# Performance work log

Hardware: AMD Instinct MI355X
Metric: run time of the kernel (lower is better)

Reference implementation:

```python
import jax, jax.numpy as jnp
import numpy as np

B, C, H, W = 4, 256, 128, 128


def setup_inputs() -> dict:
    key = jax.random.key(0)
    k1, k2, k3, k4 = jax.random.split(key, 4)
    x = jax.random.normal(k1, (B, C, H, W), dtype=jnp.float32)
    offset = jax.random.normal(k2, (B, 18, H, W), dtype=jnp.float32)
    # 1x1 conv weights, normal_init std=0.01, zero bias (mmcv normal_init default)
    w0 = jax.random.normal(k3, (C, C), dtype=jnp.float32) * 0.01
    b0 = jnp.zeros((C,), dtype=jnp.float32)
    w1 = jax.random.normal(k4, (C, C), dtype=jnp.float32) * 0.01
    b1 = jnp.zeros((C,), dtype=jnp.float32)
    return {"x": x, "offset": offset, "w0": w0, "b0": b0, "w1": w1, "b1": b1}


def _bilinear(x, py, px):
    # x: [B,C,H,W]; py,px: [B,H,W] fractional sample coords; zero outside bounds (DCN convention)
    Bb, Cc, Hh, Ww = x.shape
    y0 = jnp.floor(py)
    x0 = jnp.floor(px)
    wy = (py - y0)[:, None]  # [B,1,H,W]
    wx = (px - x0)[:, None]
    y0i = y0.astype(jnp.int32)
    x0i = x0.astype(jnp.int32)
    xf = x.reshape(Bb, Cc, Hh * Ww)

    def corner(yi, xi):
        valid = ((yi >= 0) & (yi < Hh) & (xi >= 0) & (xi < Ww)).astype(x.dtype)
        idx = (jnp.clip(yi, 0, Hh - 1) * Ww + jnp.clip(xi, 0, Ww - 1)).reshape(Bb, 1, Hh * Ww)
        v = jnp.take_along_axis(xf, idx, axis=2).reshape(Bb, Cc, Hh, Ww)
        return v * valid[:, None]

    v00 = corner(y0i, x0i)
    v01 = corner(y0i, x0i + 1)
    v10 = corner(y0i + 1, x0i)
    v11 = corner(y0i + 1, x0i + 1)
    return (v00 * (1 - wy) * (1 - wx) + v01 * (1 - wy) * wx
            + v10 * wy * (1 - wx) + v11 * wy * wx)


def _channel_norm(t):
    t = t - t.mean(axis=1, keepdims=True)
    return t / jnp.sqrt(jnp.sum(t * t, axis=1, keepdims=True) + 1e-5)


def reference(x, offset, w0, b0, w1, b1):
    Bb, Cc, Hh, Ww = x.shape
    ys = jnp.arange(Hh, dtype=x.dtype)[:, None]  # [H,1]
    xs = jnp.arange(Ww, dtype=x.dtype)[None, :]  # [1,W]
    # deformable 3x3 unfold fused with max over the 9 sample points
    q = None
    for k in range(9):
        kh, kw = k // 3 - 1, k % 3 - 1
        py = ys + kh + offset[:, 2 * k]      # [B,H,W]
        px = xs + kw + offset[:, 2 * k + 1]
        s = _bilinear(x, py, px)             # [B,C,H,W]
        q = s if q is None else jnp.maximum(q, s)
    query = jnp.einsum('oc,bchw->bohw', w0, q) + b0[None, :, None, None]
    key = jnp.einsum('oc,bchw->bohw', w1, x) + b1[None, :, None, None]
    out = jnp.sum(_channel_norm(query) * _channel_norm(key), axis=1, keepdims=True)
    return out  # [B,1,H,W]
```

## Files before the change

### kernel.cpp

```cpp
#include <hip/hip_runtime.h>
#include <math.h>
#include <float.h>

#define Bd 4
#define Cd 256
#define Hd 128
#define Wd 128
#define HW (Hd*Wd)

#define PX 128
#define KC 32
#define PXM 32
#define CSTR 264

typedef __attribute__((ext_vector_type(8))) short s16x8;
typedef __attribute__((ext_vector_type(4))) float f32x4;

__device__ __forceinline__ void bf16split(float v, ushort& h, ushort& lo_) {
  uint u = __builtin_bit_cast(uint, v);
  uint uh = u + 0x7FFFu + ((u >> 16) & 1u);
  ushort hh = (ushort)(uh >> 16);
  float hf = __builtin_bit_cast(float, (uint)hh << 16);
  float res = v - hf;
  uint r = __builtin_bit_cast(uint, res);
  uint rl = r + 0x7FFFu + ((r >> 16) & 1u);
  h = hh; lo_ = (ushort)(rl >> 16);
}

__global__ __launch_bounds__(256) void prep_w_k(
    const float* __restrict__ w0, const float* __restrict__ w1,
    ushort* __restrict__ wpk) {
  const int t    = blockIdx.x * 256 + threadIdx.x;
  const int lane = t & 63;
  const int tile = (t >> 6) & 15;
  const int kc   = (t >> 10) & 7;
  const int mat  = t >> 13;
  const float* wsrc = mat ? w1 : w0;
  const int o  = tile * 16 + (lane & 15);
  const int c0 = kc * 32 + (lane >> 4) * 8;
  ushort hi[8], lo[8];
#pragma unroll
  for (int j = 0; j < 8; ++j)
    bf16split(wsrc[o * Cd + c0 + j], hi[j], lo[j]);
  const size_t bh = ((((size_t)(mat * 2 + 0) * 8 + kc) * 16 + tile) * 64 + lane) * 8;
  const size_t bl = ((((size_t)(mat * 2 + 1) * 8 + kc) * 16 + tile) * 64 + lane) * 8;
#pragma unroll
  for (int j = 0; j < 8; ++j) { wpk[bh + j] = hi[j]; wpk[bl + j] = lo[j]; }
}

__global__ __launch_bounds__(256) void transpose_x_k(
    const float* __restrict__ x, float* __restrict__ xT) {
  __shared__ float t[32][33];
  const int b   = blockIdx.z;
  const int hw0 = blockIdx.x * 32;
  const int c0  = blockIdx.y * 32;
  const int tx = threadIdx.x & 31, ty = threadIdx.x >> 5;
  const float* xb  = x  + (size_t)b * Cd * HW;
  float*       xTb = xT + (size_t)b * HW * Cd;
#pragma unroll
  for (int i = 0; i < 32; i += 8)
    t[ty + i][tx] = xb[(size_t)(c0 + ty + i) * HW + hw0 + tx];
  __syncthreads();
#pragma unroll
  for (int i = 0; i < 32; i += 8)
    xTb[(size_t)(hw0 + ty + i) * Cd + c0 + tx] = t[tx][ty + i];
}

__device__ __forceinline__ void deform_job(
    int j, int pbase, const float* __restrict__ offb, uint* __restrict__ dstbase) {
  const int px = j / 9, k = j - px * 9;
  const int p = pbase + px;
  const int h = p >> 7, w = p & (Wd - 1);
  const float oy = offb[(2 * k) * HW + p];
  const float ox = offb[(2 * k + 1) * HW + p];
  const float py = (float)(h + k / 3 - 1) + oy;
  const float pxx = (float)(w + k % 3 - 1) + ox;
  const float y0f = floorf(py), x0f = floorf(pxx);
  const float wy = py - y0f, wx = pxx - x0f;
  const int y0 = (int)y0f, x0 = (int)x0f;
  const int y1 = y0 + 1,  x1 = x0 + 1;
  const float vy0 = (y0 >= 0 && y0 < Hd) ? 1.f : 0.f;
  const float vy1 = (y1 >= 0 && y1 < Hd) ? 1.f : 0.f;
  const float vx0 = (x0 >= 0 && x0 < Wd) ? 1.f : 0.f;
  const float vx1 = (x1 >= 0 && x1 < Wd) ? 1.f : 0.f;
  const int cy0 = min(max(y0, 0), Hd-1), cy1 = min(max(y1, 0), Hd-1);
  const int cx0 = min(max(x0, 0), Wd-1), cx1 = min(max(x1, 0), Wd-1);
  uint4 iv;
  iv.x = (uint)(cy0 * Wd + cx0) * Cd;
  iv.y = (uint)(cy0 * Wd + cx1) * Cd;
  iv.z = (uint)(cy1 * Wd + cx0) * Cd;
  iv.w = (uint)(cy1 * Wd + cx1) * Cd;
  float4 cv;
  cv.x = (1.f-wy)*(1.f-wx) * vy0*vx0;
  cv.y = (1.f-wy)*wx       * vy0*vx1;
  cv.z = wy*(1.f-wx)       * vy1*vx0;
  cv.w = wy*wx             * vy1*vx1;
  uint* d = dstbase + (size_t)(px * 9 + k) * 8;
  *(uint4*)d = iv;
  *(float4*)(d + 4) = cv;
}

__global__ __launch_bounds__(256) void merged_k(
    const float* __restrict__ xT, const float* __restrict__ off,
    const ushort* __restrict__ wpk,
    const float* __restrict__ b0, const float* __restrict__ b1,
    float* __restrict__ out) {
  __shared__ ushort act[4 * PXM * CSTR];
  __shared__ __align__(16) uint coef[4][8 * 9 * 8];

  const int bid = blockIdx.x;
  const int swz = (bid & 7) * 256 + (bid >> 3);
  const int b    = swz >> 9;
  const int tile = swz & 511;

  const int tid = threadIdx.x;
  const int l   = tid & 63, wv = tid >> 6;
  const int px0   = tile * PXM;
  const int pbase = px0 + wv * 8;

  const float* offb = off + (size_t)b * 18 * HW;

  deform_job(l, pbase, offb, &coef[wv][0]);
  if (l < 8) deform_job(64 + l, pbase, offb, &coef[wv][0]);
  __syncthreads();

  {
    const float* xTb = xT + (size_t)b * HW * Cd + l * 4;
    ushort* qh_base = act + 0 * PXM * CSTR;
    ushort* ql_base = act + 1 * PXM * CSTR;
#pragma unroll 2
    for (int pi = 0; pi < 8; ++pi) {
      float m0 = -FLT_MAX, m1 = -FLT_MAX, m2 = -FLT_MAX, m3 = -FLT_MAX;
#pragma unroll
      for (int k = 0; k < 9; ++k) {
        const uint* cp = &coef[wv][(pi * 9 + k) * 8];
        const uint4  iv = *(const uint4*)cp;
        const float4 cw = *(const float4*)(cp + 4);
        const float4 v00 = *(const float4*)(xTb + iv.x);
        const float4 v01 = *(const float4*)(xTb + iv.y);
        const float4 v10 = *(const float4*)(xTb + iv.z);
        const float4 v11 = *(const float4*)(xTb + iv.w);
        m0 = fmaxf(m0, fmaf(cw.x, v00.x, fmaf(cw.y, v01.x, fmaf(cw.z, v10.x, cw.w*v11.x))));
        m1 = fmaxf(m1, fmaf(cw.x, v00.y, fmaf(cw.y, v01.y, fmaf(cw.z, v10.y, cw.w*v11.y))));
        m2 = fmaxf(m2, fmaf(cw.x, v00.z, fmaf(cw.y, v01.z, fmaf(cw.z, v10.z, cw.w*v11.z))));
        m3 = fmaxf(m3, fmaf(cw.x, v00.w, fmaf(cw.y, v01.w, fmaf(cw.z, v10.w, cw.w*v11.w))));
      }
      ushort4 hh, ll;
      bf16split(m0, hh.x, ll.x); bf16split(m1, hh.y, ll.y);
      bf16split(m2, hh.z, ll.z); bf16split(m3, hh.w, ll.w);
      const int pl = wv * 8 + pi;
      *(ushort4*)(qh_base + pl * CSTR + l * 4) = hh;
      *(ushort4*)(ql_base + pl * CSTR + l * 4) = ll;
    }
  }

  {
    const int r  = tid >> 3;
    const int c0 = (tid & 7) * 32;
    const float* xrow = xT + ((size_t)b * HW + px0 + r) * Cd + c0;
    ushort* dx_h = act + 2 * PXM * CSTR + r * CSTR + c0;
    ushort* dx_l = act + 3 * PXM * CSTR + r * CSTR + c0;
#pragma unroll
    for (int i = 0; i < 8; ++i) {
      const float4 xv = ((const float4*)xrow)[i];
      ushort4 xh, xl;
      bf16split(xv.x, xh.x, xl.x); bf16split(xv.y, xh.y, xl.y);
      bf16split(xv.z, xh.z, xl.z); bf16split(xv.w, xh.w, xl.w);
      *(ushort4*)(dx_h + 4*i) = xh; *(ushort4*)(dx_l + 4*i) = xl;
    }
  }
  __syncthreads();

  const f32x4 z = {0.f, 0.f, 0.f, 0.f};
  f32x4 accQ[4][2], accK[4][2];
#pragma unroll
  for (int a = 0; a < 4; ++a)
#pragma unroll
    for (int bt = 0; bt < 2; ++bt) { accQ[a][bt] = z; accK[a][bt] = z; }

#pragma unroll 2
  for (int kc = 0; kc < 8; ++kc) {
    s16x8 a0h[4], a0l[4], a1h[4], a1l[4];
#pragma unroll
    for (int a = 0; a < 4; ++a) {
      const int ta = wv * 4 + a;
      a0h[a] = *(const s16x8*)(wpk + (((size_t)(0 * 8 + kc) * 16 + ta) * 64 + l) * 8);
      a0l[a] = *(const s16x8*)(wpk + (((size_t)(1 * 8 + kc) * 16 + ta) * 64 + l) * 8);
      a1h[a] = *(const s16x8*)(wpk + (((size_t)(2 * 8 + kc) * 16 + ta) * 64 + l) * 8);
      a1l[a] = *(const s16x8*)(wpk + (((size_t)(3 * 8 + kc) * 16 + ta) * 64 + l) * 8);
    }
#pragma unroll
    for (int bt = 0; bt < 2; ++bt) {
      const int row  = bt * 16 + (l & 15);
      const int coff = kc * 32 + (l >> 4) * 8;
      const ushort* base = act + row * CSTR + coff;
      const s16x8 bqh = *(const s16x8*)(base + 0 * PXM * CSTR);
      const s16x8 bql = *(const s16x8*)(base + 1 * PXM * CSTR);
      const s16x8 bxh = *(const s16x8*)(base + 2 * PXM * CSTR);
      const s16x8 bxl = *(const s16x8*)(base + 3 * PXM * CSTR);
#pragma unroll
      for (int a = 0; a < 4; ++a) {
        accQ[a][bt] = __builtin_amdgcn_mfma_f32_16x16x32_bf16(a0h[a], bqh, accQ[a][bt], 0, 0, 0);
        accQ[a][bt] = __builtin_amdgcn_mfma_f32_16x16x32_bf16(a0h[a], bql, accQ[a][bt], 0, 0, 0);
        accQ[a][bt] = __builtin_amdgcn_mfma_f32_16x16x32_bf16(a0l[a], bqh, accQ[a][bt], 0, 0, 0);
        accK[a][bt] = __builtin_amdgcn_mfma_f32_16x16x32_bf16(a1h[a], bxh, accK[a][bt], 0, 0, 0);
        accK[a][bt] = __builtin_amdgcn_mfma_f32_16x16x32_bf16(a1h[a], bxl, accK[a][bt], 0, 0, 0);
        accK[a][bt] = __builtin_amdgcn_mfma_f32_16x16x32_bf16(a1l[a], bxh, accK[a][bt], 0, 0, 0);
      }
    }
  }

  float bq[4][4], bk[4][4];
#pragma unroll
  for (int a = 0; a < 4; ++a)
#pragma unroll
    for (int r = 0; r < 4; ++r) {
      const int o = wv * 64 + a * 16 + (l >> 4) * 4 + r;
      bq[a][r] = b0[o]; bk[a][r] = b1[o];
    }

  float st[2][5];
#pragma unroll
  for (int bt = 0; bt < 2; ++bt)
#pragma unroll
    for (int s = 0; s < 5; ++s) st[bt][s] = 0.f;
#pragma unroll
  for (int bt = 0; bt < 2; ++bt)
#pragma unroll
    for (int a = 0; a < 4; ++a)
#pragma unroll
      for (int r = 0; r < 4; ++r) {
        const float Qv = accQ[a][bt][r] + bq[a][r];
        const float Kv = accK[a][bt][r] + bk[a][r];
        st[bt][0] += Qv;
        st[bt][1] += Kv;
        st[bt][2] = fmaf(Qv, Qv, st[bt][2]);
        st[bt][3] = fmaf(Kv, Kv, st[bt][3]);
        st[bt][4] = fmaf(Qv, Kv, st[bt][4]);
      }
#pragma unroll
  for (int bt = 0; bt < 2; ++bt)
#pragma unroll
    for (int s = 0; s < 5; ++s) {
      float v = st[bt][s];
      v += __shfl_xor(v, 16, 64);
      v += __shfl_xor(v, 32, 64);
      st[bt][s] = v;
    }

  __syncthreads();
  float* sl = (float*)act;
  if (l < 32) {
    const int mybt = l >> 4, col = l & 15;
#pragma unroll
    for (int s = 0; s < 5; ++s)
      sl[((wv * 32) + mybt * 16 + col) * 5 + s] = st[mybt][s];
  }
  __syncthreads();
  if (tid < PXM) {
    float sQ = 0.f, sK = 0.f, sQQ = 0.f, sKK = 0.f, sQK = 0.f;
#pragma unroll
    for (int w4 = 0; w4 < 4; ++w4) {
      const float* p = sl + ((w4 * 32) + tid) * 5;
      sQ += p[0]; sK += p[1]; sQQ += p[2]; sKK += p[3]; sQK += p[4];
    }
    const float num = sQK - sQ * sK * (1.f / 256.f);
    const float dq  = sQQ - sQ * sQ * (1.f / 256.f) + 1e-5f;
    const float dk  = sKK - sK * sK * (1.f / 256.f) + 1e-5f;
    out[(size_t)b * HW + px0 + tid] = num / sqrtf(dq * dk);
  }
}

__global__ __launch_bounds__(256) void transpose_k(
    const float* __restrict__ w0, const float* __restrict__ w1,
    float* __restrict__ w0T, float* __restrict__ w1T) {
  __shared__ float tile[32][33];
  const float* src = blockIdx.y ? w1 : w0;
  float*       dst = blockIdx.y ? w1T : w0T;
  const int bx = blockIdx.x & 7, by = blockIdx.x >> 3;
  const int tx = threadIdx.x & 31, ty = threadIdx.x >> 5;
#pragma unroll
  for (int i = 0; i < 32; i += 8)
    tile[ty + i][tx] = src[(by*32 + ty + i)*Cd + bx*32 + tx];
  __syncthreads();
#pragma unroll
  for (int i = 0; i < 32; i += 8)
    dst[(bx*32 + ty + i)*Cd + by*32 + tx] = tile[tx][ty + i];
}

__global__ __launch_bounds__(256) void deform_max_k(
    const float* __restrict__ x, const float* __restrict__ off,
    float* __restrict__ q) {
  const int b   = blockIdx.y;
  const int c0  = blockIdx.z << 5;
  const int hw0 = (blockIdx.x << 8) + threadIdx.x;
  const int h   = hw0 >> 7;
  const int w   = hw0 & (Wd - 1);
  const float* offb = off + ((size_t)b * 18) * HW + hw0;
  int   i00[9], i01[9], i10[9], i11[9];
  float c00[9], c01[9], c10[9], c11[9];
#pragma unroll
  for (int k = 0; k < 9; ++k) {
    const int kh = k / 3 - 1, kw = k % 3 - 1;
    const float oy = offb[(size_t)(2*k)   * HW];
    const float ox = offb[(size_t)(2*k+1) * HW];
    const float py = (float)(h + kh) + oy;
    const float px = (float)(w + kw) + ox;
    const float y0f = floorf(py), x0f = floorf(px);
    const float wy = py - y0f, wx = px - x0f;
    const int y0 = (int)y0f, x0 = (int)x0f;
    const int y1 = y0 + 1,  x1 = x0 + 1;
    const float vy0 = (y0 >= 0 && y0 < Hd) ? 1.f : 0.f;
    const float vy1 = (y1 >= 0 && y1 < Hd) ? 1.f : 0.f;
    const float vx0 = (x0 >= 0 && x0 < Wd) ? 1.f : 0.f;
    const float vx1 = (x1 >= 0 && x1 < Wd) ? 1.f : 0.f;
    const int cy0 = min(max(y0, 0), Hd-1), cy1 = min(max(y1, 0), Hd-1);
    const int cx0 = min(max(x0, 0), Wd-1), cx1 = min(max(x1, 0), Wd-1);
    i00[k] = cy0 * Wd + cx0;  i01[k] = cy0 * Wd + cx1;
    i10[k] = cy1 * Wd + cx0;  i11[k] = cy1 * Wd + cx1;
    c00[k] = (1.f-wy)*(1.f-wx) * vy0*vx0;
    c01[k] = (1.f-wy)*wx       * vy0*vx1;
    c10[k] = wy*(1.f-wx)       * vy1*vx0;
    c11[k] = wy*wx             * vy1*vx1;
  }
  const float* xb = x + ((size_t)(b * Cd + c0)) * HW;
  float*       qb = q + ((size_t)(b * Cd + c0)) * HW + hw0;
#pragma unroll 4
  for (int c = 0; c < 32; ++c) {
    const float* xc = xb + (size_t)c * HW;
    float m = -3.402823466e38f;
#pragma unroll
    for (int k = 0; k < 9; ++k) {
      const float s = c00[k]*xc[i00[k]] + c01[k]*xc[i01[k]]
                    + c10[k]*xc[i10[k]] + c11[k]*xc[i11[k]];
      m = fmaxf(m, s);
    }
    qb[(size_t)c * HW] = m;
  }
}

__global__ __launch_bounds__(512) void fused_k(
    const float* __restrict__ x, const float* __restrict__ q,
    const float* __restrict__ w0T, const float* __restrict__ w1T,
    const float* __restrict__ b0, const float* __restrict__ b1,
    float* __restrict__ out) {
  __shared__ float w0s[KC * 256];
  __shared__ float w1s[KC * 256];
  __shared__ float qs [KC * PX];
  __shared__ float xs [KC * PX];
  const int b    = blockIdx.y;
  const int px0  = blockIdx.x * PX;
  const int tid  = threadIdx.x;
  const int o_t  = tid & 31;
  const int px_t = tid >> 5;
  float accQ[8][8], accK[8][8];
#pragma unroll
  for (int i = 0; i < 8; ++i) {
    const int o = (i < 4) ? (4*o_t + i) : (128 + 4*o_t + (i - 4));
    const float bqv = b0[o], bkv = b1[o];
#pragma unroll
    for (int j = 0; j < 8; ++j) { accQ[i][j] = bqv; accK[i][j] = bkv; }
  }
  const float* qb = q + ((size_t)b * Cd) * HW + px0;
  const float* xb = x + ((size_t)b * Cd) * HW + px0;
  for (int kc = 0; kc < Cd; kc += KC) {
    __syncthreads();
    {
      const float4* s0 = (const float4*)(w0T + (size_t)kc * 256);
      const float4* s1 = (const float4*)(w1T + (size_t)kc * 256);
      float4* d0 = (float4*)w0s;
      float4* d1 = (float4*)w1s;
#pragma unroll
      for (int i = 0; i < 4; ++i) {
        d0[tid*4 + i] = s0[tid*4 + i];
        d1[tid*4 + i] = s1[tid*4 + i];
      }
#pragma unroll
      for (int i = 0; i < 2; ++i) {
        const int f  = tid*2 + i;
        const int cc = f >> 5, p4 = f & 31;
        ((float4*)qs)[cc*(PX/4) + p4] =
            ((const float4*)(qb + (size_t)(kc+cc) * HW))[p4];
        ((float4*)xs)[cc*(PX/4) + p4] =
            ((const float4*)(xb + (size_t)(kc+cc) * HW))[p4];
      }
    }
    __syncthreads();
#pragma unroll 4
    for (int cc = 0; cc < KC; ++cc) {
      float a0[8], a1[8], qv[8], xv[8];
      *(float4*)&a0[0] = *(const float4*)&w0s[cc*256 + 4*o_t];
      *(float4*)&a0[4] = *(const float4*)&w0s[cc*256 + 128 + 4*o_t];
      *(float4*)&a1[0] = *(const float4*)&w1s[cc*256 + 4*o_t];
      *(float4*)&a1[4] = *(const float4*)&w1s[cc*256 + 128 + 4*o_t];
      *(float4*)&qv[0] = *(const float4*)&qs[cc*PX + 8*px_t];
      *(float4*)&qv[4] = *(const float4*)&qs[cc*PX + 8*px_t + 4];
      *(float4*)&xv[0] = *(const float4*)&xs[cc*PX + 8*px_t];
      *(float4*)&xv[4] = *(const float4*)&xs[cc*PX + 8*px_t + 4];
#pragma unroll
      for (int i = 0; i < 8; ++i)
#pragma unroll
        for (int j = 0; j < 8; ++j) {
          accQ[i][j] = fmaf(a0[i], qv[j], accQ[i][j]);
          accK[i][j] = fmaf(a1[i], xv[j], accK[i][j]);
        }
    }
  }
  float outv[8];
#pragma unroll
  for (int j = 0; j < 8; ++j) {
    float sQ = 0.f, sK = 0.f, sQQ = 0.f, sKK = 0.f, sQK = 0.f;
#pragma unroll
    for (int i = 0; i < 8; ++i) {
      const float Qv = accQ[i][j], Kv = accK[i][j];
      sQ += Qv; sK += Kv;
      sQQ = fmaf(Qv, Qv, sQQ);
      sKK = fmaf(Kv, Kv, sKK);
      sQK = fmaf(Qv, Kv, sQK);
    }
#pragma unroll
    for (int m = 1; m < 32; m <<= 1) {
      sQ  += __shfl_xor(sQ,  m, 64);
      sK  += __shfl_xor(sK,  m, 64);
      sQQ += __shfl_xor(sQQ, m, 64);
      sKK += __shfl_xor(sKK, m, 64);
      sQK += __shfl_xor(sQK, m, 64);
    }
    const float num = sQK - sQ*sK*(1.f/256.f);
    const float dq  = sQQ - sQ*sQ*(1.f/256.f) + 1e-5f;
    const float dk  = sKK - sK*sK*(1.f/256.f) + 1e-5f;
    outv[j] = num / sqrtf(dq * dk);
  }
  if (o_t == 0) {
    float* ob = out + (size_t)b * HW + px0 + px_t*8;
#pragma unroll
    for (int j = 0; j < 8; ++j) ob[j] = outv[j];
  }
}

extern "C" void kernel_launch(void* const* d_in, const int* in_sizes, int n_in,
                              void* d_out, int out_size, void* d_ws, size_t ws_size,
                              hipStream_t stream) {
  const float* x   = (const float*)d_in[0];
  const float* off = (const float*)d_in[1];
  const float* w0  = (const float*)d_in[2];
  const float* b0  = (const float*)d_in[3];
  const float* w1  = (const float*)d_in[4];
  const float* b1  = (const float*)d_in[5];
  float* out = (float*)d_out;

  const size_t tensor_elems = (size_t)Bd * Cd * HW;
  const size_t wpk_bytes    = 4 * 65536 * sizeof(ushort);
  const size_t need_fast    = wpk_bytes + tensor_elems * 4;

  if (ws_size >= need_fast) {
    ushort* wpk = (ushort*)d_ws;
    float*  xT  = (float*)((char*)d_ws + wpk_bytes);
    prep_w_k     <<<64, 256, 0, stream>>>(w0, w1, wpk);
    transpose_x_k<<<dim3(HW/32, Cd/32, Bd), 256, 0, stream>>>(x, xT);
    merged_k     <<<2048, 256, 0, stream>>>(xT, off, wpk, b0, b1, out);
  } else {
    float* w0T = (float*)d_ws;
    float* w1T = w0T + 65536;
    float* qws = w1T + 65536;
    transpose_k <<<dim3(64, 2),     256, 0, stream>>>(w0, w1, w0T, w1T);
    deform_max_k<<<dim3(64, Bd, 8), 256, 0, stream>>>(x, off, qws);
    fused_k     <<<dim3(HW/PX, Bd), 512, 0, stream>>>(x, qws, w0T, w1T, b0, b1, out);
  }
}
```

Before: 281.5 us.

## Load x MFMA fragments directly from global, halve LDS, raise occupancy bound

The x tile is no longer split into bf16 hi/lo halves and staged in LDS. Each lane now loads its B-fragment for the key GEMM straight from global memory inside the k-loop and splits it in registers. This halves the LDS array, and launch bounds now request 3 blocks per CU to raise occupancy. Weight fragments are loaded per output tile inside the loop to cut live registers. The cost is redundant global loads and bf16 splits, since each x value is read by all 4 waves.

```diff
diff --git a/kernel.cpp b/kernel.cpp
--- a/kernel.cpp
+++ b/kernel.cpp
@@ -100,12 +100,12 @@
   *(float4*)(d + 4) = cv;
 }
 
-__global__ __launch_bounds__(256) void merged_k(
+__global__ __launch_bounds__(256, 3) void merged_k(
     const float* __restrict__ xT, const float* __restrict__ off,
     const ushort* __restrict__ wpk,
     const float* __restrict__ b0, const float* __restrict__ b1,
     float* __restrict__ out) {
-  __shared__ ushort act[4 * PXM * CSTR];
+  __shared__ ushort act[2 * PXM * CSTR];
   __shared__ __align__(16) uint coef[4][8 * 9 * 8];
 
   const int bid = blockIdx.x;
@@ -153,22 +153,6 @@
       *(ushort4*)(ql_base + pl * CSTR + l * 4) = ll;
     }
   }
-
-  {
-    const int r  = tid >> 3;
-    const int c0 = (tid & 7) * 32;
-    const float* xrow = xT + ((size_t)b * HW + px0 + r) * Cd + c0;
-    ushort* dx_h = act + 2 * PXM * CSTR + r * CSTR + c0;
-    ushort* dx_l = act + 3 * PXM * CSTR + r * CSTR + c0;
-#pragma unroll
-    for (int i = 0; i < 8; ++i) {
-      const float4 xv = ((const float4*)xrow)[i];
-      ushort4 xh, xl;
-      bf16split(xv.x, xh.x, xl.x); bf16split(xv.y, xh.y, xl.y);
-      bf16split(xv.z, xh.z, xl.z); bf16split(xv.w, xh.w, xl.w);
-      *(ushort4*)(dx_h + 4*i) = xh; *(ushort4*)(dx_l + 4*i) = xl;
-    }
-  }
   __syncthreads();
 
   const f32x4 z = {0.f, 0.f, 0.f, 0.f};
@@ -178,34 +162,48 @@
 #pragma unroll
     for (int bt = 0; bt < 2; ++bt) { accQ[a][bt] = z; accK[a][bt] = z; }
 
+  const float* xfrag_base = xT + ((size_t)b * HW + px0 + (l & 15)) * Cd + (l >> 4) * 8;
+
 #pragma unroll 2
   for (int kc = 0; kc < 8; ++kc) {
-    s16x8 a0h[4], a0l[4], a1h[4], a1l[4];
-#pragma unroll
-    for (int a = 0; a < 4; ++a) {
-      const int ta = wv * 4 + a;
-      a0h[a] = *(const s16x8*)(wpk + (((size_t)(0 * 8 + kc) * 16 + ta) * 64 + l) * 8);
-      a0l[a] = *(const s16x8*)(wpk + (((size_t)(1 * 8 + kc) * 16 + ta) * 64 + l) * 8);
-      a1h[a] = *(const s16x8*)(wpk + (((size_t)(2 * 8 + kc) * 16 + ta) * 64 + l) * 8);
-      a1l[a] = *(const s16x8*)(wpk + (((size_t)(3 * 8 + kc) * 16 + ta) * 64 + l) * 8);
-    }
+    s16x8 bxh[2], bxl[2];
+#pragma unroll
+    for (int bt = 0; bt < 2; ++bt) {
+      const float* xr = xfrag_base + (size_t)(bt * 16) * Cd + kc * 32;
+      const float4 xa = *(const float4*)xr;
+      const float4 xb4 = *(const float4*)(xr + 4);
+      ushort h[8], lo[8];
+      bf16split(xa.x,  h[0], lo[0]); bf16split(xa.y,  h[1], lo[1]);
+      bf16split(xa.z,  h[2], lo[2]); bf16split(xa.w,  h[3], lo[3]);
+      bf16split(xb4.x, h[4], lo[4]); bf16split(xb4.y, h[5], lo[5]);
+      bf16split(xb4.z, h[6], lo[6]); bf16split(xb4.w, h[7], lo[7]);
+#pragma unroll
+      for (int j = 0; j < 8; ++j) { bxh[bt][j] = (short)h[j]; bxl[bt][j] = (short)lo[j]; }
+    }
+    s16x8 bqh[2], bql[2];
 #pragma unroll
     for (int bt = 0; bt < 2; ++bt) {
       const int row  = bt * 16 + (l & 15);
       const int coff = kc * 32 + (l >> 4) * 8;
       const ushort* base = act + row * CSTR + coff;
-      const s16x8 bqh = *(const s16x8*)(base + 0 * PXM * CSTR);
-      const s16x8 bql = *(const s16x8*)(base + 1 * PXM * CSTR);
-      const s16x8 bxh = *(const s16x8*)(base + 2 * PXM * CSTR);
-      const s16x8 bxl = *(const s16x8*)(base + 3 * PXM * CSTR);
-#pragma unroll
-      for (int a = 0; a < 4; ++a) {
-        accQ[a][bt] = __builtin_amdgcn_mfma_f32_16x16x32_bf16(a0h[a], bqh, accQ[a][bt], 0, 0, 0);
-        accQ[a][bt] = __builtin_amdgcn_mfma_f32_16x16x32_bf16(a0h[a], bql, accQ[a][bt], 0, 0, 0);
-        accQ[a][bt] = __builtin_amdgcn_mfma_f32_16x16x32_bf16(a0l[a], bqh, accQ[a][bt], 0, 0, 0);
-        accK[a][bt] = __builtin_amdgcn_mfma_f32_16x16x32_bf16(a1h[a], bxh, accK[a][bt], 0, 0, 0);
-        accK[a][bt] = __builtin_amdgcn_mfma_f32_16x16x32_bf16(a1h[a], bxl, accK[a][bt], 0, 0, 0);
-        accK[a][bt] = __builtin_amdgcn_mfma_f32_16x16x32_bf16(a1l[a], bxh, accK[a][bt], 0, 0, 0);
+      bqh[bt] = *(const s16x8*)(base + 0 * PXM * CSTR);
+      bql[bt] = *(const s16x8*)(base + 1 * PXM * CSTR);
+    }
+#pragma unroll
+    for (int a = 0; a < 4; ++a) {
+      const int ta = wv * 4 + a;
+      const s16x8 a0h = *(const s16x8*)(wpk + (((size_t)(0 * 8 + kc) * 16 + ta) * 64 + l) * 8);
+      const s16x8 a0l = *(const s16x8*)(wpk + (((size_t)(1 * 8 + kc) * 16 + ta) * 64 + l) * 8);
+      const s16x8 a1h = *(const s16x8*)(wpk + (((size_t)(2 * 8 + kc) * 16 + ta) * 64 + l) * 8);
+      const s16x8 a1l = *(const s16x8*)(wpk + (((size_t)(3 * 8 + kc) * 16 + ta) * 64 + l) * 8);
+#pragma unroll
+      for (int bt = 0; bt < 2; ++bt) {
+        accQ[a][bt] = __builtin_amdgcn_mfma_f32_16x16x32_bf16(a0h, bqh[bt], accQ[a][bt], 0, 0, 0);
+        accQ[a][bt] = __builtin_amdgcn_mfma_f32_16x16x32_bf16(a0h, bql[bt], accQ[a][bt], 0, 0, 0);
+        accQ[a][bt] = __builtin_amdgcn_mfma_f32_16x16x32_bf16(a0l, bqh[bt], accQ[a][bt], 0, 0, 0);
+        accK[a][bt] = __builtin_amdgcn_mfma_f32_16x16x32_bf16(a1h, bxh[bt], accK[a][bt], 0, 0, 0);
+        accK[a][bt] = __builtin_amdgcn_mfma_f32_16x16x32_bf16(a1h, bxl[bt], accK[a][bt], 0, 0, 0);
+        accK[a][bt] = __builtin_amdgcn_mfma_f32_16x16x32_bf16(a1l, bxh[bt], accK[a][bt], 0, 0, 0);
       }
     }
   }
```

Result: slower. 333.7 us (+18.6%).
